# Optimization experiments

Measured on AMD Instinct MI355X. Metric: run time of the kernel, lower is better.

The kernel has to match this reference:

```python
import jax, jax.numpy as jnp
import numpy as np

N = 8192          # total nodes in batch
D_IN = 64         # input feature dim
D_H = 64          # hidden dim
D_OUT = 10        # num classes
B = 64            # number of graphs (idx in [0, B))
NUM_ITERS = 5     # power iterations for rs-pool
VALUE_ALPHA = 1.0
EPS = 0.0         # GIN eps (train_eps=False)


def setup_inputs() -> dict:
    key = jax.random.key(0)
    ks = jax.random.split(key, 8)
    x_in = jax.random.normal(ks[0], (N, D_IN), dtype=jnp.float32)
    a = (jax.random.uniform(ks[1], (N, N)) < 0.005).astype(jnp.float32)
    adj = jnp.maximum(a, a.T)
    idx = (jnp.arange(N) // (N // B)).astype(jnp.int32)  # 64 graphs x 128 nodes
    s1 = 1.0 / np.sqrt(D_IN)
    s2 = 1.0 / np.sqrt(D_H)
    W1 = jax.random.uniform(ks[2], (D_IN, D_H), minval=-s1, maxval=s1, dtype=jnp.float32)
    b1 = jax.random.uniform(ks[3], (D_H,), minval=-s1, maxval=s1, dtype=jnp.float32)
    W2 = jax.random.uniform(ks[4], (D_H, D_H), minval=-s2, maxval=s2, dtype=jnp.float32)
    b2 = jax.random.uniform(ks[5], (D_H,), minval=-s2, maxval=s2, dtype=jnp.float32)
    Wl = jax.random.uniform(ks[6], (D_H, D_OUT), minval=-s2, maxval=s2, dtype=jnp.float32)
    bl = jax.random.uniform(ks[7], (D_OUT,), minval=-s2, maxval=s2, dtype=jnp.float32)
    return {"x_in": x_in, "adj": adj, "idx": idx,
            "W1": W1, "b1": b1, "W2": W2, "b2": b2, "Wl": Wl, "bl": bl}


def reference(x_in, adj, idx, W1, b1, W2, b2, Wl, bl):
    n = adj.shape[0]
    A = adj + jnp.eye(n, dtype=adj.dtype)  # self-loops added in forward
    # GINConv: aggregate (A@x + eps*x) then linear + ReLU
    h = jax.nn.relu((A @ x_in + EPS * x_in) @ W1 + b1)   # [N, D_H]
    h = jax.nn.relu((A @ h + EPS * h) @ W2 + b2)         # [N, D_H]

    seg = lambda v: jax.ops.segment_sum(v, idx, num_segments=B)

    # rs-pool: batched power iteration for dominant right singular vector per graph
    vec = seg(h)                                                   # [B, D_H]
    vec = vec / (jnp.linalg.norm(vec, axis=1, keepdims=True) + 1e-8)
    for _ in range(NUM_ITERS):
        y = jnp.sum(h * vec[idx], axis=1, keepdims=True)           # X_g @ v_g, per node
        vec = seg(y * h)                                           # X_g^T (X_g v_g)
        vec = vec / (jnp.linalg.norm(vec, axis=1, keepdims=True) + 1e-8)
    y = jnp.sum(h * vec[idx], axis=1)                              # [N]
    sv = jnp.sqrt(seg(y * y))                                      # ||X_g v_g|| per graph [B]
    pooled = vec * (sv / VALUE_ALPHA)[:, None]                     # [B, D_H]

    out = pooled @ Wl + bl                                         # [B, D_OUT]
    return jax.nn.log_softmax(out, axis=1)
```

## Files before the change

### kernel.cpp

```cpp
#include <hip/hip_runtime.h>
#include <math.h>

#define NN 8192
#define DH 64
#define DOUT 10
#define NG 64
#define NPG 128
#define NITER 5
#define TPAD 160
#define NCHUNK (NN * NN / 256)

typedef float f32x4 __attribute__((ext_vector_type(4)));
typedef unsigned long long u64;
typedef u64 u64x2 __attribute__((ext_vector_type(2)));

__global__ __launch_bounds__(256) void scan_bitmap(
    const float* __restrict__ adj, u64* __restrict__ bmp)
{
    const int lane = threadIdx.x & 63;
    const int gw   = (blockIdx.x * 256 + threadIdx.x) >> 6;
    const int nw   = (gridDim.x * 256) >> 6;
    #pragma unroll 4
    for (int g = gw; g < NCHUNK; g += nw) {
        f32x4 a4 = *reinterpret_cast<const f32x4*>(adj + (size_t)g * 256 + lane * 4);
        u64 m0 = __ballot(a4.x != 0.0f);
        u64 m1 = __ballot(a4.y != 0.0f);
        u64 m2 = __ballot(a4.z != 0.0f);
        u64 m3 = __ballot(a4.w != 0.0f);
        u64 msel = (lane & 2) ? ((lane & 1) ? m3 : m2)
                              : ((lane & 1) ? m1 : m0);
        if (lane < 4) bmp[(size_t)g * 4 + lane] = msel;
    }
}

__global__ __launch_bounds__(256) void gin_layer(
    const float* __restrict__ x, const u64* __restrict__ bmp,
    const float* __restrict__ W, const float* __restrict__ bias,
    float* __restrict__ out)
{
    __shared__ float sW[DH * DH];
    __shared__ unsigned short sJ[4][TPAD];
    __shared__ float sAccF[4][DH];

    for (int t = threadIdx.x; t < DH * DH; t += 256) sW[t] = W[t];
    __syncthreads();

    const int wave = threadIdx.x >> 6;
    const int lane = threadIdx.x & 63;
    const int row  = blockIdx.x * 4 + wave;

    const u64* brow = bmp + (size_t)row * (NN / 64);
    u64x2 wp = *reinterpret_cast<const u64x2*>(brow + 2 * lane);
    u64 w0 = wp.x, w1 = wp.y;
    int cnt = __popcll(w0) + __popcll(w1);

    int p = cnt;
    #pragma unroll
    for (int off = 1; off < 64; off <<= 1) {
        int t = __shfl_up(p, off);
        if (lane >= off) p += t;
    }
    int pos  = p - cnt;
    int ctot = __shfl(p, 63);

    {
        int widx = 2 * lane;
        int base0 = (widx >> 2) * 256 + (widx & 3);
        while (w0) { int b = __ffsll(w0) - 1; w0 &= w0 - 1;
                     sJ[wave][pos++] = (unsigned short)(base0 + 4 * b); }
        int widx1 = 2 * lane + 1;
        int base1 = (widx1 >> 2) * 256 + (widx1 & 3);
        while (w1) { int b = __ffsll(w1) - 1; w1 &= w1 - 1;
                     sJ[wave][pos++] = (unsigned short)(base1 + 4 * b); }
    }
    for (int e = ctot + lane; e < TPAD; e += 64) sJ[wave][e] = 0;

    float acc = x[row * DH + lane];
    const int tmax = (ctot + 15) & ~15;
    #pragma unroll 1
    for (int e0 = 0; e0 < tmax; e0 += 16) {
        int jj[16];
        float vv[16];
        #pragma unroll
        for (int s = 0; s < 16; ++s) jj[s] = sJ[wave][e0 + s];
        #pragma unroll
        for (int s = 0; s < 16; ++s) vv[s] = x[jj[s] * DH + lane];
        #pragma unroll
        for (int s = 0; s < 16; ++s)
            acc += (e0 + s < ctot) ? vv[s] : 0.0f;
    }

    sAccF[wave][lane] = acc;
    float o = bias[lane];
    #pragma unroll
    for (int k = 0; k < DH; ++k) o += sAccF[wave][k] * sW[k * DH + lane];
    out[row * DH + lane] = fmaxf(o, 0.0f);
}

__global__ __launch_bounds__(256) void rspool_head(
    const float* __restrict__ h, const float* __restrict__ Wl,
    const float* __restrict__ bl, float* __restrict__ out)
{
    __shared__ float sX[NPG * 65];
    __shared__ float sY[NPG];
    __shared__ float sVec[DH];
    __shared__ float sPart[4][DH];
    __shared__ float sPooled[DH];
    __shared__ float sO[DOUT];

    const int g = blockIdx.x;
    const int d = threadIdx.x & 63;
    const int q = threadIdx.x >> 6;

    const float* hg = h + (size_t)g * NPG * DH;
    for (int t = threadIdx.x; t < NPG * DH; t += 256)
        sX[(t >> 6) * 65 + (t & 63)] = hg[t];
    __syncthreads();

    {
        float p = 0.0f;
        for (int i = q * 32; i < q * 32 + 32; ++i) p += sX[i * 65 + d];
        sPart[q][d] = p;
    }
    __syncthreads();
    if (threadIdx.x < 64) {
        float v = sPart[0][d] + sPart[1][d] + sPart[2][d] + sPart[3][d];
        float s = v * v;
        #pragma unroll
        for (int off = 32; off > 0; off >>= 1) s += __shfl_xor(s, off);
        sVec[d] = v / (sqrtf(s) + 1e-8f);
    }
    __syncthreads();

    for (int it = 0; it < NITER; ++it) {
        if (threadIdx.x < NPG) {
            int i = threadIdx.x;
            float yy = 0.0f;
            #pragma unroll
            for (int dd = 0; dd < DH; ++dd) yy += sX[i * 65 + dd] * sVec[dd];
            sY[i] = yy;
        }
        __syncthreads();
        {
            float p = 0.0f;
            for (int i = q * 32; i < q * 32 + 32; ++i) p += sY[i] * sX[i * 65 + d];
            sPart[q][d] = p;
        }
        __syncthreads();
        if (threadIdx.x < 64) {
            float v = sPart[0][d] + sPart[1][d] + sPart[2][d] + sPart[3][d];
            float s = v * v;
            #pragma unroll
            for (int off = 32; off > 0; off >>= 1) s += __shfl_xor(s, off);
            sVec[d] = v / (sqrtf(s) + 1e-8f);
        }
        __syncthreads();
    }

    if (threadIdx.x < NPG) {
        int i = threadIdx.x;
        float yy = 0.0f;
        #pragma unroll
        for (int dd = 0; dd < DH; ++dd) yy += sX[i * 65 + dd] * sVec[dd];
        sY[i] = yy;
    }
    __syncthreads();
    if (threadIdx.x < 64) {
        float s = sY[d] * sY[d] + sY[64 + d] * sY[64 + d];
        #pragma unroll
        for (int off = 32; off > 0; off >>= 1) s += __shfl_xor(s, off);
        float sv = sqrtf(s);
        sPooled[d] = sVec[d] * sv;
    }
    __syncthreads();

    if (threadIdx.x < DOUT) {
        int c = threadIdx.x;
        float o = bl[c];
        #pragma unroll
        for (int dd = 0; dd < DH; ++dd) o += sPooled[dd] * Wl[dd * DOUT + c];
        sO[c] = o;
    }
    __syncthreads();
    if (threadIdx.x < DOUT) {
        int c = threadIdx.x;
        float mx = -INFINITY;
        #pragma unroll
        for (int j = 0; j < DOUT; ++j) mx = fmaxf(mx, sO[j]);
        float se = 0.0f;
        #pragma unroll
        for (int j = 0; j < DOUT; ++j) se += expf(sO[j] - mx);
        out[g * DOUT + c] = sO[c] - mx - logf(se);
    }
}

extern "C" void kernel_launch(void* const* d_in, const int* in_sizes, int n_in,
                              void* d_out, int out_size, void* d_ws, size_t ws_size,
                              hipStream_t stream) {
    const float* x_in = (const float*)d_in[0];
    const float* adj  = (const float*)d_in[1];
    const float* W1 = (const float*)d_in[3];
    const float* b1 = (const float*)d_in[4];
    const float* W2 = (const float*)d_in[5];
    const float* b2 = (const float*)d_in[6];
    const float* Wl = (const float*)d_in[7];
    const float* bl = (const float*)d_in[8];
    float* out = (float*)d_out;

    char* ws = (char*)d_ws;
    float* h1 = (float*)ws;
    float* h2 = h1 + NN * DH;
    u64*   bmp = (u64*)(ws + 8 * 1024 * 1024);

    scan_bitmap<<<2048, 256, 0, stream>>>(adj, bmp);
    gin_layer<<<NN / 4, 256, 0, stream>>>(x_in, bmp, W1, b1, h1);
    gin_layer<<<NN / 4, 256, 0, stream>>>(h1, bmp, W2, b2, h2);
    rspool_head<<<NG, 256, 0, stream>>>(h2, Wl, bl, out);
}
```

Before: 89.01 us.

## Process two rows per wave in GIN layer and widen bitmap scan loads

The GIN layer now has each wave handle two adjacent rows. Their neighbor gathers are interleaved in chunks of eight, with 128-bit LDS index loads, and the final 64x64 linear uses readlane broadcasts instead of a shared-memory round trip. This amortizes the weight load and the block setup over twice as many rows and gives more independent loads per iteration. The bitmap scan processes two 256-float chunks per wave iteration to raise memory-level parallelism. The costs are more registers per thread (launch bounds set to 4 blocks), half as many blocks, and divergence when the two rows have different degrees.

Measured after the change: 91.37 us. 2.7% more time.

```diff
diff --git a/kernel.cpp b/kernel.cpp
--- a/kernel.cpp
+++ b/kernel.cpp
@@ -20,81 +20,121 @@
     const int lane = threadIdx.x & 63;
     const int gw   = (blockIdx.x * 256 + threadIdx.x) >> 6;
     const int nw   = (gridDim.x * 256) >> 6;
-    #pragma unroll 4
-    for (int g = gw; g < NCHUNK; g += nw) {
-        f32x4 a4 = *reinterpret_cast<const f32x4*>(adj + (size_t)g * 256 + lane * 4);
-        u64 m0 = __ballot(a4.x != 0.0f);
-        u64 m1 = __ballot(a4.y != 0.0f);
-        u64 m2 = __ballot(a4.z != 0.0f);
-        u64 m3 = __ballot(a4.w != 0.0f);
-        u64 msel = (lane & 2) ? ((lane & 1) ? m3 : m2)
-                              : ((lane & 1) ? m1 : m0);
-        if (lane < 4) bmp[(size_t)g * 4 + lane] = msel;
-    }
-}
-
-__global__ __launch_bounds__(256) void gin_layer(
+    const int npair = NCHUNK / 2;
+    #pragma unroll 2
+    for (int pp = gw; pp < npair; pp += nw) {
+        const float* base = adj + (size_t)pp * 512;
+        f32x4 a = *reinterpret_cast<const f32x4*>(base + lane * 4);
+        f32x4 b = *reinterpret_cast<const f32x4*>(base + 256 + lane * 4);
+        u64 a0 = __ballot(a.x != 0.0f);
+        u64 a1 = __ballot(a.y != 0.0f);
+        u64 a2 = __ballot(a.z != 0.0f);
+        u64 a3 = __ballot(a.w != 0.0f);
+        u64 b0 = __ballot(b.x != 0.0f);
+        u64 b1 = __ballot(b.y != 0.0f);
+        u64 b2 = __ballot(b.z != 0.0f);
+        u64 b3 = __ballot(b.w != 0.0f);
+        u64 selA = (lane & 2) ? ((lane & 1) ? a3 : a2) : ((lane & 1) ? a1 : a0);
+        u64 selB = (lane & 2) ? ((lane & 1) ? b3 : b2) : ((lane & 1) ? b1 : b0);
+        u64 w = (lane & 4) ? selB : selA;
+        if (lane < 8) bmp[(size_t)pp * 8 + lane] = w;
+    }
+}
+
+__global__ __launch_bounds__(256, 4) void gin_layer(
     const float* __restrict__ x, const u64* __restrict__ bmp,
     const float* __restrict__ W, const float* __restrict__ bias,
     float* __restrict__ out)
 {
     __shared__ float sW[DH * DH];
-    __shared__ unsigned short sJ[4][TPAD];
-    __shared__ float sAccF[4][DH];
+    __shared__ unsigned short sJ[4][2][TPAD];
 
     for (int t = threadIdx.x; t < DH * DH; t += 256) sW[t] = W[t];
     __syncthreads();
 
     const int wave = threadIdx.x >> 6;
     const int lane = threadIdx.x & 63;
-    const int row  = blockIdx.x * 4 + wave;
-
-    const u64* brow = bmp + (size_t)row * (NN / 64);
-    u64x2 wp = *reinterpret_cast<const u64x2*>(brow + 2 * lane);
-    u64 w0 = wp.x, w1 = wp.y;
-    int cnt = __popcll(w0) + __popcll(w1);
-
-    int p = cnt;
+    const int wgid = blockIdx.x * 4 + wave;
+
+    int ctotR[2];
     #pragma unroll
-    for (int off = 1; off < 64; off <<= 1) {
-        int t = __shfl_up(p, off);
-        if (lane >= off) p += t;
-    }
-    int pos  = p - cnt;
-    int ctot = __shfl(p, 63);
-
-    {
+    for (int r = 0; r < 2; ++r) {
+        const int row = wgid * 2 + r;
+        const u64* brow = bmp + (size_t)row * (NN / 64);
+        u64x2 wp = *reinterpret_cast<const u64x2*>(brow + 2 * lane);
+        u64 w0 = wp.x, w1 = wp.y;
+        int cnt = __popcll(w0) + __popcll(w1);
+
+        int p = cnt;
+        #pragma unroll
+        for (int off = 1; off < 64; off <<= 1) {
+            int t = __shfl_up(p, off);
+            if (lane >= off) p += t;
+        }
+        int pos  = p - cnt;
+        int ctot = __shfl(p, 63);
+
         int widx = 2 * lane;
         int base0 = (widx >> 2) * 256 + (widx & 3);
         while (w0) { int b = __ffsll(w0) - 1; w0 &= w0 - 1;
-                     sJ[wave][pos++] = (unsigned short)(base0 + 4 * b); }
+                     sJ[wave][r][pos++] = (unsigned short)(base0 + 4 * b); }
         int widx1 = 2 * lane + 1;
         int base1 = (widx1 >> 2) * 256 + (widx1 & 3);
         while (w1) { int b = __ffsll(w1) - 1; w1 &= w1 - 1;
-                     sJ[wave][pos++] = (unsigned short)(base1 + 4 * b); }
-    }
-    for (int e = ctot + lane; e < TPAD; e += 64) sJ[wave][e] = 0;
-
-    float acc = x[row * DH + lane];
-    const int tmax = (ctot + 15) & ~15;
+                     sJ[wave][r][pos++] = (unsigned short)(base1 + 4 * b); }
+
+        for (int e = ctot + lane; e < TPAD; e += 64) sJ[wave][r][e] = 0;
+        ctotR[r] = ctot;
+    }
+
+    const int rowA = wgid * 2, rowB = wgid * 2 + 1;
+    const int ctotA = ctotR[0], ctotB = ctotR[1];
+
+    float accA = x[rowA * DH + lane];
+    float accB = x[rowB * DH + lane];
+    const int tmaxA = (ctotA + 7) & ~7;
+    const int tmaxB = (ctotB + 7) & ~7;
+    const int tmax  = tmaxA > tmaxB ? tmaxA : tmaxB;
     #pragma unroll 1
-    for (int e0 = 0; e0 < tmax; e0 += 16) {
-        int jj[16];
-        float vv[16];
-        #pragma unroll
-        for (int s = 0; s < 16; ++s) jj[s] = sJ[wave][e0 + s];
-        #pragma unroll
-        for (int s = 0; s < 16; ++s) vv[s] = x[jj[s] * DH + lane];
-        #pragma unroll
-        for (int s = 0; s < 16; ++s)
-            acc += (e0 + s < ctot) ? vv[s] : 0.0f;
-    }
-
-    sAccF[wave][lane] = acc;
-    float o = bias[lane];
+    for (int e0 = 0; e0 < tmax; e0 += 8) {
+        uint4 ja = *reinterpret_cast<const uint4*>(&sJ[wave][0][e0]);
+        uint4 jb = *reinterpret_cast<const uint4*>(&sJ[wave][1][e0]);
+        unsigned jA[8], jB[8];
+        jA[0] = ja.x & 0xffffu; jA[1] = ja.x >> 16;
+        jA[2] = ja.y & 0xffffu; jA[3] = ja.y >> 16;
+        jA[4] = ja.z & 0xffffu; jA[5] = ja.z >> 16;
+        jA[6] = ja.w & 0xffffu; jA[7] = ja.w >> 16;
+        jB[0] = jb.x & 0xffffu; jB[1] = jb.x >> 16;
+        jB[2] = jb.y & 0xffffu; jB[3] = jb.y >> 16;
+        jB[4] = jb.z & 0xffffu; jB[5] = jb.z >> 16;
+        jB[6] = jb.w & 0xffffu; jB[7] = jb.w >> 16;
+        float vA[8], vB[8];
+        #pragma unroll
+        for (int s = 0; s < 8; ++s) vA[s] = x[jA[s] * DH + lane];
+        #pragma unroll
+        for (int s = 0; s < 8; ++s) vB[s] = x[jB[s] * DH + lane];
+        #pragma unroll
+        for (int s = 0; s < 8; ++s)
+            accA += (e0 + s < ctotA) ? vA[s] : 0.0f;
+        #pragma unroll
+        for (int s = 0; s < 8; ++s)
+            accB += (e0 + s < ctotB) ? vB[s] : 0.0f;
+    }
+
+    float oA = bias[lane];
+    float oB = oA;
     #pragma unroll
-    for (int k = 0; k < DH; ++k) o += sAccF[wave][k] * sW[k * DH + lane];
-    out[row * DH + lane] = fmaxf(o, 0.0f);
+    for (int k = 0; k < DH; ++k) {
+        float wk = sW[k * DH + lane];
+        float aAk = __int_as_float(
+            __builtin_amdgcn_readlane(__float_as_int(accA), k));
+        float aBk = __int_as_float(
+            __builtin_amdgcn_readlane(__float_as_int(accB), k));
+        oA = fmaf(aAk, wk, oA);
+        oB = fmaf(aBk, wk, oB);
+    }
+    out[rowA * DH + lane] = fmaxf(oA, 0.0f);
+    out[rowB * DH + lane] = fmaxf(oB, 0.0f);
 }
 
 __global__ __launch_bounds__(256) void rspool_head(
@@ -213,7 +253,7 @@
     u64*   bmp = (u64*)(ws + 8 * 1024 * 1024);
 
     scan_bitmap<<<2048, 256, 0, stream>>>(adj, bmp);
-    gin_layer<<<NN / 4, 256, 0, stream>>>(x_in, bmp, W1, b1, h1);
-    gin_layer<<<NN / 4, 256, 0, stream>>>(h1, bmp, W2, b2, h2);
+    gin_layer<<<NN / 8, 256, 0, stream>>>(x_in, bmp, W1, b1, h1);
+    gin_layer<<<NN / 8, 256, 0, stream>>>(h1, bmp, W2, b2, h2);
     rspool_head<<<NG, 256, 0, stream>>>(h2, Wl, bl, out);
 }
```
